# Kernel optimization log

Measured on AMD Instinct MI355X. Metric: run time of the kernel, lower is better.

Reference implementation:

```python
import jax, jax.numpy as jnp
import numpy as np

B, CIN, H, W = 4, 128, 160, 160
K = 100          # num instances
CH = 8           # mask head channels
OUT = 8          # mask branch out channels
STRIDE = 4
EPS = 1e-5


def conv3x3(x, w):
    # x: [B,C,H,W], w: [O,C,3,3] -> [B,O,H,W], stride 1, pad 1
    return jax.lax.conv_general_dilated(x, w, (1, 1), 'SAME',
                                        dimension_numbers=('NCHW', 'OIHW', 'NCHW'))


def setup_inputs() -> dict:
    key = jax.random.key(0)
    ks = jax.random.split(key, 6)
    cnn_feature = jax.random.normal(ks[0], (B, CIN, H, W), jnp.float32)
    tower_w = jax.random.normal(ks[1], (4, 128, 128, 3, 3), jnp.float32) * 0.03
    bn_gamma = jnp.ones((4, 128), jnp.float32)
    bn_beta = jnp.zeros((4, 128), jnp.float32)
    bn_mean = jnp.zeros((4, 128), jnp.float32)
    bn_var = jnp.ones((4, 128), jnp.float32)
    proj_w = jax.random.normal(ks[2], (OUT, 128), jnp.float32) * 0.05
    proj_b = jnp.zeros((OUT,), jnp.float32)
    ctrl_w = jax.random.normal(ks[3], (169, CIN, 3, 3), jnp.float32) * 0.01
    ctrl_b = jnp.zeros((169,), jnp.float32)
    detection = jax.random.randint(ks[4], (K, 2), 0, min(H, W), dtype=jnp.int32)
    return dict(cnn_feature=cnn_feature, tower_w=tower_w, bn_gamma=bn_gamma,
                bn_beta=bn_beta, bn_mean=bn_mean, bn_var=bn_var,
                proj_w=proj_w, proj_b=proj_b, ctrl_w=ctrl_w, ctrl_b=ctrl_b,
                detection=detection)


def reference(cnn_feature, tower_w, bn_gamma, bn_beta, bn_mean, bn_var,
              proj_w, proj_b, ctrl_w, ctrl_b, detection):
    x = cnn_feature
    for i in range(4):
        x = conv3x3(x, tower_w[i])
        inv = bn_gamma[i] / jnp.sqrt(bn_var[i] + EPS)            # [128]
        shift = bn_beta[i] - bn_mean[i] * inv
        x = jax.nn.relu(x * inv[None, :, None, None] + shift[None, :, None, None])
    mask_feats = jnp.einsum('bchw,oc->bohw', x, proj_w) + proj_b[None, :, None, None]

    # ----- controller: 3x3 conv producing 169 dynamic params per pixel -----
    ctrl = conv3x3(cnn_feature, ctrl_w) + ctrl_b[None, :, None, None]  # [B,169,H,W]

    # ----- gather per-instance params at detection centers (im_inds all 0) -----
    xs = detection[:, 0]
    ys = detection[:, 1]
    params = ctrl[0][:, ys, xs].T  # [K,169]

    # ----- relative coordinates -----
    sx = jnp.arange(W, dtype=jnp.float32) * STRIDE + STRIDE // 2
    sy = jnp.arange(H, dtype=jnp.float32) * STRIDE + STRIDE // 2
    gy, gx = jnp.meshgrid(sy, sx, indexing='ij')
    locations = jnp.stack([gx.reshape(-1), gy.reshape(-1)], axis=1)   # [HW,2]
    ct = detection.astype(jnp.float32) * STRIDE                        # [K,2]
    rel = (ct[:, None, :] - locations[None, :, :]).transpose(0, 2, 1)  # [K,2,HW]

    feats = jnp.broadcast_to(mask_feats[0].reshape(1, OUT, H * W), (K, OUT, H * W))
    h = jnp.concatenate([rel, feats], axis=1)  # [K,10,HW]

    # ----- parse dynamic params: weights first, then biases -----
    w0 = params[:, 0:80].reshape(K, CH, OUT + 2)     # (8+2)*8
    w1 = params[:, 80:144].reshape(K, CH, CH)        # 8*8
    w2 = params[:, 144:152].reshape(K, 1, CH)        # 8*1
    b0 = params[:, 152:160]
    b1 = params[:, 160:168]
    b2 = params[:, 168:169]

    # ----- dynamic grouped 1x1 convs == per-instance matmuls -----
    h = jax.nn.relu(jnp.einsum('koc,kcp->kop', w0, h) + b0[:, :, None])
    h = jax.nn.relu(jnp.einsum('koc,kcp->kop', w1, h) + b1[:, :, None])
    h = jnp.einsum('koc,kcp->kop', w2, h) + b2[:, :, None]  # [K,1,HW]
    return h.reshape(K, H, W)
```

## Files before the change

### kernel.cpp

```cpp
#include <hip/hip_runtime.h>
#include <hip/hip_bf16.h>

#define H 160
#define W 160
#define HW 25600
#define ROWB 40960

typedef __attribute__((ext_vector_type(8))) short bf16x8;
typedef __attribute__((ext_vector_type(4))) float f32x4;
typedef __attribute__((ext_vector_type(8))) unsigned short ushort8v;
typedef __attribute__((ext_vector_type(4))) unsigned short ushort4v;

typedef __attribute__((address_space(1))) const unsigned int gu32;
typedef __attribute__((address_space(3))) unsigned int lu32;

__device__ __forceinline__ void gload16(const void* g, void* l) {
    __builtin_amdgcn_global_load_lds((gu32*)g, (lu32*)l, 16, 0, 0);
}

__device__ __forceinline__ unsigned short f2b(float f) {
    unsigned int u = __float_as_uint(f);
    unsigned int r = (u + 0x7fffu + ((u >> 16) & 1u)) >> 16;
    return (unsigned short)r;
}
__device__ __forceinline__ float b2f(unsigned short b) {
    return __uint_as_float(((unsigned int)b) << 16);
}

#define LGKM0() asm volatile("s_waitcnt lgkmcnt(0)" ::: "memory")
#define BARRIER() asm volatile("s_barrier" ::: "memory")


__global__ __launch_bounds__(256) void prep_weights(
    const float* __restrict__ tw,
    const float* __restrict__ gamma, const float* __restrict__ beta,
    const float* __restrict__ mean,  const float* __restrict__ var,
    char* __restrict__ wbf, float* __restrict__ invshift)
{
    int idx = blockIdx.x * 256 + threadIdx.x;
    int ci = idx & 127;
    int co = (idx >> 7) & 127;
    int lt = idx >> 14;
    int l  = lt / 9;
    int tap = lt - l * 9;
    int kk = ci >> 5;
    int cw = ci & 31;
    float v = tw[(((l * 128 + co) * 128 + ci) * 9) + tap];
    *(unsigned short*)(wbf + (lt * 4 + kk) * 8192 + co * 64 + cw * 2) = f2b(v);

    if (blockIdx.x == 0) {
        for (int c = threadIdx.x; c < 512; c += 256) {
            int ll = c >> 7, ch = c & 127;
            float inv = gamma[ll * 128 + ch] * rsqrtf(var[ll * 128 + ch] + 1e-5f);
            float sh  = beta[ll * 128 + ch] - mean[ll * 128 + ch] * inv;
            invshift[ll * 256 + ch] = inv;
            invshift[ll * 256 + 128 + ch] = sh;
        }
    }
}

__global__ __launch_bounds__(256) void prep_input(
    const float* __restrict__ cnn, char* __restrict__ actX)
{
    int idx = blockIdx.x * 256 + threadIdx.x;
    int cb = idx & 15;
    int p  = idx >> 4;
    int x  = p % W;
    int key = (x & 7) << 5;
    int ci0 = cb * 8;
    ushort8v o;
#pragma unroll
    for (int j = 0; j < 8; ++j)
        o[j] = f2b(cnn[(ci0 + j) * HW + p]);
    *(ushort8v*)(actX + p * 256 + ((cb * 16) ^ key)) = o;
}

template <int PROJ>
__global__ __launch_bounds__(256, 2) void conv_mfma(
    const char* __restrict__ actin,
    const char* __restrict__ wpl,
    const float* __restrict__ invshift_l,
    char* __restrict__ actout,
    const float* __restrict__ pw,
    const float* __restrict__ pb,
    float* __restrict__ mf)
{
    __shared__ __align__(16) char smem[60416];
    char* IT = smem;
    char* WQ = smem + 27648;

    const int tid  = threadIdx.x;
    const int lane = tid & 63;
    const int wave = tid >> 6;
    const int g    = lane >> 4;
    const int i15  = lane & 15;
    const int wc   = wave >> 1;
    const int wp   = wave & 1;

    const int bx = blockIdx.x;
    const int by = blockIdx.y;
    const int tx0 = bx * 16 - 1;
    const int ty0 = by * 4 - 1;

    for (int it = 0; it < 7; ++it) {
        int c = it * 256 + tid;
        if (c < 1728) {
            int row  = c / 288;
            int rem  = c - row * 288;
            int px_i = rem >> 4;
            int bo   = (rem & 15) * 16;
            int cy = min(max(ty0 + row, 0), H - 1);
            int cx = min(max(tx0 + px_i, 0), W - 1);
            char* ldsb = IT + (it * 256 + (tid & ~63)) * 16;
            gload16(actin + cy * ROWB + cx * 256 + bo, ldsb);
        }
    }
#pragma unroll
    for (int pl = 0; pl < 3; ++pl) {
        const char* src = wpl + pl * 8192;
        char* dst = WQ + pl * 8192;
        gload16(src + (0 * 256 + tid) * 16, dst + (0 * 256 + (tid & ~63)) * 16);
        gload16(src + (1 * 256 + tid) * 16, dst + (1 * 256 + (tid & ~63)) * 16);
    }
    asm volatile("s_waitcnt vmcnt(6)" ::: "memory");
    for (int c = tid; c < 1728; c += 256) {
        int row  = c / 288;
        int rem  = c - row * 288;
        int px_i = rem >> 4;
        int gy = ty0 + row, gx = tx0 + px_i;
        if ((unsigned)gy >= (unsigned)H || (unsigned)gx >= (unsigned)W) {
            f32x4 z = {0.f, 0.f, 0.f, 0.f};
            *(f32x4*)(IT + c * 16) = z;
        }
    }
    LGKM0();
    BARRIER();

    f32x4 acc[4][2];
#pragma unroll
    for (int cf = 0; cf < 4; ++cf)
#pragma unroll
        for (int pf = 0; pf < 2; ++pf)
            acc[cf][pf] = (f32x4){0.f, 0.f, 0.f, 0.f};

#define CSTAGE(J, WN) {                                                        \
    if ((J) <= 32) {                                                           \
        const char* src = wpl + ((J) + 3) * 8192;                              \
        char* dst = WQ + (((J) + 3) & 3) * 8192;                               \
        gload16(src + (0*256 + tid) * 16, dst + (0*256 + (tid & ~63)) * 16);   \
        gload16(src + (1*256 + tid) * 16, dst + (1*256 + (tid & ~63)) * 16);   \
    }                                                                          \
    asm volatile("s_waitcnt vmcnt(" #WN ")" ::: "memory");                     \
    {                                                                          \
        const int tap = (J) >> 2, kk = (J) & 3;                                \
        const int r = tap / 3, s = tap - r * 3;                                \
        const int kb = kk * 64 + g * 16;                                       \
        const int keyb = ((i15 + s + 7) & 7) << 5;                             \
        const char* wbase = WQ + ((J) & 3) * 8192 + (wc * 64 + i15) * 64 + g * 16; \
        bf16x8 a0 = *(const bf16x8*)(wbase + 0 * 1024);                        \
        bf16x8 a1 = *(const bf16x8*)(wbase + 1 * 1024);                        \
        bf16x8 a2 = *(const bf16x8*)(wbase + 2 * 1024);                        \
        bf16x8 a3 = *(const bf16x8*)(wbase + 3 * 1024);                        \
        const char* ib = IT + (i15 + s) * 256 + (kb ^ keyb);                   \
        bf16x8 b0 = *(const bf16x8*)(ib + (wp * 2 + 0 + r) * 4608);            \
        bf16x8 b1 = *(const bf16x8*)(ib + (wp * 2 + 1 + r) * 4608);            \
        acc[0][0] = __builtin_amdgcn_mfma_f32_16x16x32_bf16(a0, b0, acc[0][0], 0, 0, 0); \
        acc[0][1] = __builtin_amdgcn_mfma_f32_16x16x32_bf16(a0, b1, acc[0][1], 0, 0, 0); \
        acc[1][0] = __builtin_amdgcn_mfma_f32_16x16x32_bf16(a1, b0, acc[1][0], 0, 0, 0); \
        acc[1][1] = __builtin_amdgcn_mfma_f32_16x16x32_bf16(a1, b1, acc[1][1], 0, 0, 0); \
        acc[2][0] = __builtin_amdgcn_mfma_f32_16x16x32_bf16(a2, b0, acc[2][0], 0, 0, 0); \
        acc[2][1] = __builtin_amdgcn_mfma_f32_16x16x32_bf16(a2, b1, acc[2][1], 0, 0, 0); \
        acc[3][0] = __builtin_amdgcn_mfma_f32_16x16x32_bf16(a3, b0, acc[3][0], 0, 0, 0); \
        acc[3][1] = __builtin_amdgcn_mfma_f32_16x16x32_bf16(a3, b1, acc[3][1], 0, 0, 0); \
    }                                                                          \
    BARRIER();                                                                 \
}

    CSTAGE(0,4)  CSTAGE(1,4)  CSTAGE(2,4)  CSTAGE(3,4)  CSTAGE(4,4)  CSTAGE(5,4)
    CSTAGE(6,4)  CSTAGE(7,4)  CSTAGE(8,4)  CSTAGE(9,4)  CSTAGE(10,4) CSTAGE(11,4)
    CSTAGE(12,4) CSTAGE(13,4) CSTAGE(14,4) CSTAGE(15,4) CSTAGE(16,4) CSTAGE(17,4)
    CSTAGE(18,4) CSTAGE(19,4) CSTAGE(20,4) CSTAGE(21,4) CSTAGE(22,4) CSTAGE(23,4)
    CSTAGE(24,4) CSTAGE(25,4) CSTAGE(26,4) CSTAGE(27,4) CSTAGE(28,4) CSTAGE(29,4)
    CSTAGE(30,4) CSTAGE(31,4) CSTAGE(32,4) CSTAGE(33,2) CSTAGE(34,0) CSTAGE(35,0)
#undef CSTAGE

    if (PROJ == 0) {
        const int gx = bx * 16 + i15;
        const int keyo = (gx & 7) << 5;
#pragma unroll
        for (int cf = 0; cf < 4; ++cf) {
            int co0 = wc * 64 + cf * 16 + g * 4;
            f32x4 inv4 = *(const f32x4*)&invshift_l[co0];
            f32x4 sh4  = *(const f32x4*)&invshift_l[128 + co0];
#pragma unroll
            for (int pf = 0; pf < 2; ++pf) {
                int gy = by * 4 + wp * 2 + pf;
                f32x4 v = acc[cf][pf];
                ushort4v o;
                o.x = f2b(fmaxf(v.x * inv4.x + sh4.x, 0.f));
                o.y = f2b(fmaxf(v.y * inv4.y + sh4.y, 0.f));
                o.z = f2b(fmaxf(v.z * inv4.z + sh4.z, 0.f));
                o.w = f2b(fmaxf(v.w * inv4.w + sh4.w, 0.f));
                *(ushort4v*)(actout + gy * ROWB + gx * 256 + ((co0 * 2) ^ keyo)) = o;
            }
        }
    } else {
        float* actF = (float*)(smem + 27648);
        float* spw  = (float*)smem;
#pragma unroll
        for (int cf = 0; cf < 4; ++cf) {
            int co0 = wc * 64 + cf * 16 + g * 4;
            f32x4 inv4 = *(const f32x4*)&invshift_l[co0];
            f32x4 sh4  = *(const f32x4*)&invshift_l[128 + co0];
#pragma unroll
            for (int pf = 0; pf < 2; ++pf) {
                int pxi = (wp * 2 + pf) * 16 + i15;
                f32x4 v = acc[cf][pf];
                f32x4 o;
                o.x = fmaxf(v.x * inv4.x + sh4.x, 0.f);
                o.y = fmaxf(v.y * inv4.y + sh4.y, 0.f);
                o.z = fmaxf(v.z * inv4.z + sh4.z, 0.f);
                o.w = fmaxf(v.w * inv4.w + sh4.w, 0.f);
                *(f32x4*)&actF[pxi * 128 + (co0 ^ ((pxi & 7) << 2))] = o;
            }
        }
        for (int i = tid; i < 1024; i += 256) spw[i] = pw[i];
        LGKM0();
        BARRIER();
        int pxt = tid >> 2;
        int o0  = (tid & 3) * 2;
        float s0 = 0.f, s1 = 0.f;
#pragma unroll
        for (int ci = 0; ci < 128; ci += 4) {
            f32x4 a  = *(const f32x4*)&actF[pxt * 128 + (ci ^ ((pxt & 7) << 2))];
            f32x4 w0 = *(const f32x4*)&spw[o0 * 128 + ci];
            f32x4 w1 = *(const f32x4*)&spw[(o0 + 1) * 128 + ci];
            s0 += a.x * w0.x + a.y * w0.y + a.z * w0.z + a.w * w0.w;
            s1 += a.x * w1.x + a.y * w1.y + a.z * w1.z + a.w * w1.w;
        }
        int p = (by * 4 + (pxt >> 4)) * W + bx * 16 + (pxt & 15);
        mf[o0 * HW + p]       = s0 + pb[o0];
        mf[(o0 + 1) * HW + p] = s1 + pb[o0 + 1];
    }
}

__global__ __launch_bounds__(256) void ctrl_kernel(
    const float* __restrict__ feat, const float* __restrict__ cw,
    const float* __restrict__ cb, const int* __restrict__ det,
    float* __restrict__ params)
{
    __shared__ float patch[1152];
    const int tid = threadIdx.x;
    const int k = blockIdx.x;
    const int xk = det[2 * k];
    const int yk = det[2 * k + 1];

    for (int i = tid; i < 1152; i += 256) {
        int ci = i / 9;
        int rem = i - ci * 9;
        int r = rem / 3, s = rem - r * 3;
        int gy = yk + r - 1, gx = xk + s - 1;
        float v = 0.f;
        if ((unsigned)gy < (unsigned)H && (unsigned)gx < (unsigned)W)
            v = feat[ci * HW + gy * W + gx];
        patch[i] = v;
    }
    __syncthreads();

    if (tid < 169) {
        float acc = cb[tid];
        const float4* cw4 = (const float4*)&cw[tid * 1152];
        const float4* p4  = (const float4*)patch;
        for (int i = 0; i < 288; ++i) {
            float4 a = p4[i];
            float4 b = cw4[i];
            acc += a.x * b.x + a.y * b.y + a.z * b.z + a.w * b.w;
        }
        params[k * 169 + tid] = acc;
    }
}

__global__ __launch_bounds__(256) void head_kernel(
    const float* __restrict__ mf, const float* __restrict__ params,
    const int* __restrict__ det, float* __restrict__ out)
{
    __shared__ float sp[1690];
    __shared__ int sdet[20];
    const int tid = threadIdx.x;
    const int kg = blockIdx.y;
    for (int i = tid; i < 1690; i += 256) sp[i] = params[kg * 1690 + i];
    if (tid < 20) sdet[tid] = det[kg * 20 + tid];
    __syncthreads();

    const int p = blockIdx.x * 256 + tid;
    const int x = p % W;
    const int y = p / W;
    const float fx = (float)(x * 4 + 2);
    const float fy = (float)(y * 4 + 2);

    float f[8];
#pragma unroll
    for (int o = 0; o < 8; ++o) f[o] = mf[o * HW + p];

#pragma unroll 2
    for (int j = 0; j < 10; ++j) {
        const float* spj = &sp[j * 169];
        const float rel0 = (float)(sdet[2 * j] * 4) - fx;
        const float rel1 = (float)(sdet[2 * j + 1] * 4) - fy;
        float h0[8];
#pragma unroll
        for (int o = 0; o < 8; ++o) {
            float a = spj[152 + o] + spj[o * 10] * rel0 + spj[o * 10 + 1] * rel1;
#pragma unroll
            for (int c = 0; c < 8; ++c) a += spj[o * 10 + 2 + c] * f[c];
            h0[o] = fmaxf(a, 0.f);
        }
        float h1[8];
#pragma unroll
        for (int o = 0; o < 8; ++o) {
            float a = spj[160 + o];
#pragma unroll
            for (int c = 0; c < 8; ++c) a += spj[80 + o * 8 + c] * h0[c];
            h1[o] = fmaxf(a, 0.f);
        }
        float r = spj[168];
#pragma unroll
        for (int c = 0; c < 8; ++c) r += spj[144 + c] * h1[c];
        out[(kg * 10 + j) * HW + p] = r;
    }
}

extern "C" void kernel_launch(void* const* d_in, const int* in_sizes, int n_in,
                              void* d_out, int out_size, void* d_ws, size_t ws_size,
                              hipStream_t stream)
{
    const float* cnn    = (const float*)d_in[0];
    const float* towerw = (const float*)d_in[1];
    const float* gamma  = (const float*)d_in[2];
    const float* beta   = (const float*)d_in[3];
    const float* meanp  = (const float*)d_in[4];
    const float* varp   = (const float*)d_in[5];
    const float* projw  = (const float*)d_in[6];
    const float* projb  = (const float*)d_in[7];
    const float* ctrlw  = (const float*)d_in[8];
    const float* ctrlb  = (const float*)d_in[9];
    const int*   det    = (const int*)d_in[10];
    float* out = (float*)d_out;

    char*  outb     = (char*)d_out;
    char*  X        = outb;
    char*  wbf      = outb + 6553600;
    float* invshift = (float*)(outb + 7733248);

    char*  Y      = (char*)d_ws;
    float* mf     = (float*)((char*)d_ws + 6553600);
    float* params = (float*)((char*)d_ws + 7372800);

    const dim3 blk(256);

    prep_weights<<<dim3(2304), blk, 0, stream>>>(towerw, gamma, beta, meanp, varp,
                                                 wbf, invshift);
    prep_input<<<dim3(1600), blk, 0, stream>>>(cnn, X);

    const dim3 cgrid(10, 40);
    conv_mfma<0><<<cgrid, blk, 0, stream>>>(X, wbf + 0 * 294912, invshift + 0 * 256,
                                            Y, nullptr, nullptr, nullptr);
    conv_mfma<0><<<cgrid, blk, 0, stream>>>(Y, wbf + 1 * 294912, invshift + 1 * 256,
                                            X, nullptr, nullptr, nullptr);
    conv_mfma<0><<<cgrid, blk, 0, stream>>>(X, wbf + 2 * 294912, invshift + 2 * 256,
                                            Y, nullptr, nullptr, nullptr);
    conv_mfma<1><<<cgrid, blk, 0, stream>>>(Y, wbf + 3 * 294912, invshift + 3 * 256,
                                            nullptr, projw, projb, mf);

    ctrl_kernel<<<dim3(100), blk, 0, stream>>>(cnn, ctrlw, ctrlb, det, params);
    head_kernel<<<dim3(100, 10), blk, 0, stream>>>(mf, params, det, out);
}
```

Before: 123.7 us.

## Split conv K-dimension across waves with per-tap weight staging and LDS reduction

The conv kernel now has each wave own a 32-channel slice of the input and compute all 128 output channels by 64 pixels. Weights for a full tap (32 KB) are staged per step, which replaces 36 fine-grained stages with 9 barriers. Partial sums are reduced across waves through LDS, and the projection epilogue is switched to bf16. This removes barrier overhead and raises MFMA density per wave, at the cost of 128 accumulator registers, dropping the 2-blocks occupancy hint, adding a reduction phase, and exposing weight loads because they are no longer double-buffered. Weight prep also loops over the 9 taps per thread with fewer blocks.

New measurement: 456.2 us. 3.69x slower.

```diff
diff --git a/kernel.cpp b/kernel.cpp
--- a/kernel.cpp
+++ b/kernel.cpp
@@ -40,13 +40,14 @@
     int idx = blockIdx.x * 256 + threadIdx.x;
     int ci = idx & 127;
     int co = (idx >> 7) & 127;
-    int lt = idx >> 14;
-    int l  = lt / 9;
-    int tap = lt - l * 9;
+    int l  = idx >> 14;
     int kk = ci >> 5;
     int cw = ci & 31;
-    float v = tw[(((l * 128 + co) * 128 + ci) * 9) + tap];
-    *(unsigned short*)(wbf + (lt * 4 + kk) * 8192 + co * 64 + cw * 2) = f2b(v);
+    const float* src = tw + ((l * 128 + co) * 128 + ci) * 9;
+    char* dst = wbf + l * 294912 + kk * 8192 + co * 64 + cw * 2;
+#pragma unroll
+    for (int t = 0; t < 9; ++t)
+        *(unsigned short*)(dst + t * 32768) = f2b(src[t]);
 
     if (blockIdx.x == 0) {
         for (int c = threadIdx.x; c < 512; c += 256) {
@@ -76,7 +77,7 @@
 }
 
 template <int PROJ>
-__global__ __launch_bounds__(256, 2) void conv_mfma(
+__global__ __launch_bounds__(256) void conv_mfma(
     const char* __restrict__ actin,
     const char* __restrict__ wpl,
     const float* __restrict__ invshift_l,
@@ -87,15 +88,13 @@
 {
     __shared__ __align__(16) char smem[60416];
     char* IT = smem;
-    char* WQ = smem + 27648;
+    char* WT = smem + 27648;
 
     const int tid  = threadIdx.x;
     const int lane = tid & 63;
-    const int wave = tid >> 6;
+    const int w    = tid >> 6;
     const int g    = lane >> 4;
     const int i15  = lane & 15;
-    const int wc   = wave >> 1;
-    const int wp   = wave & 1;
 
     const int bx = blockIdx.x;
     const int by = blockIdx.y;
@@ -116,13 +115,11 @@
         }
     }
 #pragma unroll
-    for (int pl = 0; pl < 3; ++pl) {
-        const char* src = wpl + pl * 8192;
-        char* dst = WQ + pl * 8192;
-        gload16(src + (0 * 256 + tid) * 16, dst + (0 * 256 + (tid & ~63)) * 16);
-        gload16(src + (1 * 256 + tid) * 16, dst + (1 * 256 + (tid & ~63)) * 16);
-    }
-    asm volatile("s_waitcnt vmcnt(6)" ::: "memory");
+    for (int it = 0; it < 8; ++it) {
+        int c = it * 256 + tid;
+        gload16(wpl + c * 16, WT + (it * 256 + (tid & ~63)) * 16);
+    }
+    asm volatile("s_waitcnt vmcnt(8)" ::: "memory");
     for (int c = tid; c < 1728; c += 256) {
         int row  = c / 288;
         int rem  = c - row * 288;
@@ -133,115 +130,146 @@
             *(f32x4*)(IT + c * 16) = z;
         }
     }
-    LGKM0();
-    BARRIER();
-
-    f32x4 acc[4][2];
-#pragma unroll
-    for (int cf = 0; cf < 4; ++cf)
-#pragma unroll
-        for (int pf = 0; pf < 2; ++pf)
+
+    f32x4 acc[8][4];
+#pragma unroll
+    for (int cf = 0; cf < 8; ++cf)
+#pragma unroll
+        for (int pf = 0; pf < 4; ++pf)
             acc[cf][pf] = (f32x4){0.f, 0.f, 0.f, 0.f};
 
-#define CSTAGE(J, WN) {                                                        \
-    if ((J) <= 32) {                                                           \
-        const char* src = wpl + ((J) + 3) * 8192;                              \
-        char* dst = WQ + (((J) + 3) & 3) * 8192;                               \
-        gload16(src + (0*256 + tid) * 16, dst + (0*256 + (tid & ~63)) * 16);   \
-        gload16(src + (1*256 + tid) * 16, dst + (1*256 + (tid & ~63)) * 16);   \
-    }                                                                          \
-    asm volatile("s_waitcnt vmcnt(" #WN ")" ::: "memory");                     \
-    {                                                                          \
-        const int tap = (J) >> 2, kk = (J) & 3;                                \
-        const int r = tap / 3, s = tap - r * 3;                                \
-        const int kb = kk * 64 + g * 16;                                       \
-        const int keyb = ((i15 + s + 7) & 7) << 5;                             \
-        const char* wbase = WQ + ((J) & 3) * 8192 + (wc * 64 + i15) * 64 + g * 16; \
-        bf16x8 a0 = *(const bf16x8*)(wbase + 0 * 1024);                        \
-        bf16x8 a1 = *(const bf16x8*)(wbase + 1 * 1024);                        \
-        bf16x8 a2 = *(const bf16x8*)(wbase + 2 * 1024);                        \
-        bf16x8 a3 = *(const bf16x8*)(wbase + 3 * 1024);                        \
-        const char* ib = IT + (i15 + s) * 256 + (kb ^ keyb);                   \
-        bf16x8 b0 = *(const bf16x8*)(ib + (wp * 2 + 0 + r) * 4608);            \
-        bf16x8 b1 = *(const bf16x8*)(ib + (wp * 2 + 1 + r) * 4608);            \
-        acc[0][0] = __builtin_amdgcn_mfma_f32_16x16x32_bf16(a0, b0, acc[0][0], 0, 0, 0); \
-        acc[0][1] = __builtin_amdgcn_mfma_f32_16x16x32_bf16(a0, b1, acc[0][1], 0, 0, 0); \
-        acc[1][0] = __builtin_amdgcn_mfma_f32_16x16x32_bf16(a1, b0, acc[1][0], 0, 0, 0); \
-        acc[1][1] = __builtin_amdgcn_mfma_f32_16x16x32_bf16(a1, b1, acc[1][1], 0, 0, 0); \
-        acc[2][0] = __builtin_amdgcn_mfma_f32_16x16x32_bf16(a2, b0, acc[2][0], 0, 0, 0); \
-        acc[2][1] = __builtin_amdgcn_mfma_f32_16x16x32_bf16(a2, b1, acc[2][1], 0, 0, 0); \
-        acc[3][0] = __builtin_amdgcn_mfma_f32_16x16x32_bf16(a3, b0, acc[3][0], 0, 0, 0); \
-        acc[3][1] = __builtin_amdgcn_mfma_f32_16x16x32_bf16(a3, b1, acc[3][1], 0, 0, 0); \
-    }                                                                          \
-    BARRIER();                                                                 \
-}
-
-    CSTAGE(0,4)  CSTAGE(1,4)  CSTAGE(2,4)  CSTAGE(3,4)  CSTAGE(4,4)  CSTAGE(5,4)
-    CSTAGE(6,4)  CSTAGE(7,4)  CSTAGE(8,4)  CSTAGE(9,4)  CSTAGE(10,4) CSTAGE(11,4)
-    CSTAGE(12,4) CSTAGE(13,4) CSTAGE(14,4) CSTAGE(15,4) CSTAGE(16,4) CSTAGE(17,4)
-    CSTAGE(18,4) CSTAGE(19,4) CSTAGE(20,4) CSTAGE(21,4) CSTAGE(22,4) CSTAGE(23,4)
-    CSTAGE(24,4) CSTAGE(25,4) CSTAGE(26,4) CSTAGE(27,4) CSTAGE(28,4) CSTAGE(29,4)
-    CSTAGE(30,4) CSTAGE(31,4) CSTAGE(32,4) CSTAGE(33,2) CSTAGE(34,0) CSTAGE(35,0)
-#undef CSTAGE
-
-    if (PROJ == 0) {
-        const int gx = bx * 16 + i15;
-        const int keyo = (gx & 7) << 5;
-#pragma unroll
-        for (int cf = 0; cf < 4; ++cf) {
-            int co0 = wc * 64 + cf * 16 + g * 4;
-            f32x4 inv4 = *(const f32x4*)&invshift_l[co0];
-            f32x4 sh4  = *(const f32x4*)&invshift_l[128 + co0];
-#pragma unroll
-            for (int pf = 0; pf < 2; ++pf) {
-                int gy = by * 4 + wp * 2 + pf;
-                f32x4 v = acc[cf][pf];
-                ushort4v o;
-                o.x = f2b(fmaxf(v.x * inv4.x + sh4.x, 0.f));
-                o.y = f2b(fmaxf(v.y * inv4.y + sh4.y, 0.f));
-                o.z = f2b(fmaxf(v.z * inv4.z + sh4.z, 0.f));
-                o.w = f2b(fmaxf(v.w * inv4.w + sh4.w, 0.f));
-                *(ushort4v*)(actout + gy * ROWB + gx * 256 + ((co0 * 2) ^ keyo)) = o;
-            }
-        }
-    } else {
-        float* actF = (float*)(smem + 27648);
-        float* spw  = (float*)smem;
-#pragma unroll
-        for (int cf = 0; cf < 4; ++cf) {
-            int co0 = wc * 64 + cf * 16 + g * 4;
-            f32x4 inv4 = *(const f32x4*)&invshift_l[co0];
-            f32x4 sh4  = *(const f32x4*)&invshift_l[128 + co0];
-#pragma unroll
-            for (int pf = 0; pf < 2; ++pf) {
-                int pxi = (wp * 2 + pf) * 16 + i15;
-                f32x4 v = acc[cf][pf];
-                f32x4 o;
-                o.x = fmaxf(v.x * inv4.x + sh4.x, 0.f);
-                o.y = fmaxf(v.y * inv4.y + sh4.y, 0.f);
-                o.z = fmaxf(v.z * inv4.z + sh4.z, 0.f);
-                o.w = fmaxf(v.w * inv4.w + sh4.w, 0.f);
-                *(f32x4*)&actF[pxi * 128 + (co0 ^ ((pxi & 7) << 2))] = o;
-            }
-        }
-        for (int i = tid; i < 1024; i += 256) spw[i] = pw[i];
+    const int kb = w * 64 + g * 16;
+
+#pragma unroll
+    for (int tap = 0; tap < 9; ++tap) {
+        asm volatile("s_waitcnt vmcnt(0)" ::: "memory");
         LGKM0();
         BARRIER();
-        int pxt = tid >> 2;
-        int o0  = (tid & 3) * 2;
+        {
+            const int r = tap / 3, s = tap - r * 3;
+            const int keyb = ((i15 + s + 7) & 7) << 5;
+            const char* wb = WT + w * 8192 + i15 * 64 + g * 16;
+            bf16x8 a[8];
+#pragma unroll
+            for (int cf = 0; cf < 8; ++cf)
+                a[cf] = *(const bf16x8*)(wb + cf * 1024);
+            const char* ib = IT + (i15 + s) * 256 + (kb ^ keyb);
+            bf16x8 b[4];
+#pragma unroll
+            for (int pf = 0; pf < 4; ++pf)
+                b[pf] = *(const bf16x8*)(ib + (pf + r) * 4608);
+#pragma unroll
+            for (int cf = 0; cf < 8; ++cf)
+#pragma unroll
+                for (int pf = 0; pf < 4; ++pf)
+                    acc[cf][pf] = __builtin_amdgcn_mfma_f32_16x16x32_bf16(
+                        a[cf], b[pf], acc[cf][pf], 0, 0, 0);
+        }
+        BARRIER();
+        if (tap < 8) {
+            const char* wtap = wpl + (tap + 1) * 32768;
+#pragma unroll
+            for (int it = 0; it < 8; ++it) {
+                int c = it * 256 + tid;
+                gload16(wtap + c * 16, WT + (it * 256 + (tid & ~63)) * 16);
+            }
+        }
+    }
+
+    char* redA = smem + 27648;
+    char* redB = smem + 27648 + 16384;
+    const int swz = (i15 & 7) << 4;
+#define REDAB(buf, pfi, cf) ((buf) + ((pfi) * 16 + i15) * 512 + (((cf) * 64 + g * 16) ^ swz))
+    if (w == 2) { for (int cf = 0; cf < 8; ++cf) { *(f32x4*)REDAB(redA,0,cf) = acc[cf][0]; *(f32x4*)REDAB(redA,1,cf) = acc[cf][1]; } }
+    if (w == 3) { for (int cf = 0; cf < 8; ++cf) { *(f32x4*)REDAB(redB,0,cf) = acc[cf][0]; *(f32x4*)REDAB(redB,1,cf) = acc[cf][1]; } }
+    __syncthreads();
+    if (w == 0) { for (int cf = 0; cf < 8; ++cf) { acc[cf][0] += *(f32x4*)REDAB(redA,0,cf); acc[cf][1] += *(f32x4*)REDAB(redA,1,cf); } }
+    if (w == 1) { for (int cf = 0; cf < 8; ++cf) { acc[cf][0] += *(f32x4*)REDAB(redB,0,cf); acc[cf][1] += *(f32x4*)REDAB(redB,1,cf); } }
+    __syncthreads();
+    if (w == 2) { for (int cf = 0; cf < 8; ++cf) { *(f32x4*)REDAB(redA,0,cf) = acc[cf][2]; *(f32x4*)REDAB(redA,1,cf) = acc[cf][3]; } }
+    if (w == 3) { for (int cf = 0; cf < 8; ++cf) { *(f32x4*)REDAB(redB,0,cf) = acc[cf][2]; *(f32x4*)REDAB(redB,1,cf) = acc[cf][3]; } }
+    __syncthreads();
+    if (w == 0) { for (int cf = 0; cf < 8; ++cf) { acc[cf][2] += *(f32x4*)REDAB(redA,0,cf); acc[cf][3] += *(f32x4*)REDAB(redA,1,cf); } }
+    if (w == 1) { for (int cf = 0; cf < 8; ++cf) { acc[cf][2] += *(f32x4*)REDAB(redB,0,cf); acc[cf][3] += *(f32x4*)REDAB(redB,1,cf); } }
+    __syncthreads();
+#define REDC(buf, pf, cfq) ((buf) + ((pf) * 16 + i15) * 256 + (((cfq) * 64 + g * 16) ^ swz))
+    if (w == 1) { for (int cf = 0; cf < 4; ++cf) for (int pf = 0; pf < 4; ++pf) *(f32x4*)REDC(redA, pf, cf) = acc[cf][pf]; }
+    if (w == 0) { for (int cf = 4; cf < 8; ++cf) for (int pf = 0; pf < 4; ++pf) *(f32x4*)REDC(redB, pf, (cf - 4)) = acc[cf][pf]; }
+    __syncthreads();
+    if (w == 0) { for (int cf = 0; cf < 4; ++cf) for (int pf = 0; pf < 4; ++pf) acc[cf][pf] += *(f32x4*)REDC(redA, pf, cf); }
+    if (w == 1) { for (int cf = 4; cf < 8; ++cf) for (int pf = 0; pf < 4; ++pf) acc[cf][pf] += *(f32x4*)REDC(redB, pf, (cf - 4)); }
+
+    if (PROJ == 0) {
+        if (w < 2) {
+            const int gx = bx * 16 + i15;
+            const int keyo = (gx & 7) << 5;
+            const int cf0 = w * 4;
+#pragma unroll
+            for (int cfq = 0; cfq < 4; ++cfq) {
+                int cf = cf0 + cfq;
+                int co0 = cf * 16 + g * 4;
+                f32x4 inv4 = *(const f32x4*)&invshift_l[co0];
+                f32x4 sh4  = *(const f32x4*)&invshift_l[128 + co0];
+#pragma unroll
+                for (int pf = 0; pf < 4; ++pf) {
+                    int gy = by * 4 + pf;
+                    f32x4 v = acc[cf][pf];
+                    ushort4v o;
+                    o.x = f2b(fmaxf(v.x * inv4.x + sh4.x, 0.f));
+                    o.y = f2b(fmaxf(v.y * inv4.y + sh4.y, 0.f));
+                    o.z = f2b(fmaxf(v.z * inv4.z + sh4.z, 0.f));
+                    o.w = f2b(fmaxf(v.w * inv4.w + sh4.w, 0.f));
+                    *(ushort4v*)(actout + gy * ROWB + gx * 256 + ((co0 * 2) ^ keyo)) = o;
+                }
+            }
+        }
+    } else {
+        char* actF = smem;
+        float* spw = (float*)(smem + 16384);
+        for (int i = tid; i < 1024; i += 256) spw[i] = pw[i];
+        if (w < 2) {
+            const int cf0 = w * 4;
+#pragma unroll
+            for (int cfq = 0; cfq < 4; ++cfq) {
+                int cf = cf0 + cfq;
+                int co0 = cf * 16 + g * 4;
+                f32x4 inv4 = *(const f32x4*)&invshift_l[co0];
+                f32x4 sh4  = *(const f32x4*)&invshift_l[128 + co0];
+#pragma unroll
+                for (int pf = 0; pf < 4; ++pf) {
+                    int px = pf * 16 + i15;
+                    f32x4 v = acc[cf][pf];
+                    ushort4v o;
+                    o.x = f2b(fmaxf(v.x * inv4.x + sh4.x, 0.f));
+                    o.y = f2b(fmaxf(v.y * inv4.y + sh4.y, 0.f));
+                    o.z = f2b(fmaxf(v.z * inv4.z + sh4.z, 0.f));
+                    o.w = f2b(fmaxf(v.w * inv4.w + sh4.w, 0.f));
+                    *(ushort4v*)(actF + px * 256 + ((co0 * 2) ^ ((px & 7) << 5))) = o;
+                }
+            }
+        }
+        __syncthreads();
+        int px = tid & 63;
+        int o0 = (tid >> 6) * 2;
+        int key = (px & 7) << 5;
         float s0 = 0.f, s1 = 0.f;
 #pragma unroll
-        for (int ci = 0; ci < 128; ci += 4) {
-            f32x4 a  = *(const f32x4*)&actF[pxt * 128 + (ci ^ ((pxt & 7) << 2))];
-            f32x4 w0 = *(const f32x4*)&spw[o0 * 128 + ci];
-            f32x4 w1 = *(const f32x4*)&spw[(o0 + 1) * 128 + ci];
-            s0 += a.x * w0.x + a.y * w0.y + a.z * w0.z + a.w * w0.w;
-            s1 += a.x * w1.x + a.y * w1.y + a.z * w1.z + a.w * w1.w;
-        }
-        int p = (by * 4 + (pxt >> 4)) * W + bx * 16 + (pxt & 15);
+        for (int cb = 0; cb < 16; ++cb) {
+            ushort8v vv = *(const ushort8v*)(actF + px * 256 + ((cb * 16) ^ key));
+#pragma unroll
+            for (int j = 0; j < 8; ++j) {
+                float f = b2f(vv[j]);
+                int ci = cb * 8 + j;
+                s0 += f * spw[o0 * 128 + ci];
+                s1 += f * spw[(o0 + 1) * 128 + ci];
+            }
+        }
+        int p = (by * 4 + (px >> 4)) * W + bx * 16 + (px & 15);
         mf[o0 * HW + p]       = s0 + pb[o0];
         mf[(o0 + 1) * HW + p] = s1 + pb[o0 + 1];
     }
+#undef REDAB
+#undef REDC
 }
 
 __global__ __launch_bounds__(256) void ctrl_kernel(
@@ -358,8 +386,8 @@
 
     const dim3 blk(256);
 
-    prep_weights<<<dim3(2304), blk, 0, stream>>>(towerw, gamma, beta, meanp, varp,
-                                                 wbf, invshift);
+    prep_weights<<<dim3(256), blk, 0, stream>>>(towerw, gamma, beta, meanp, varp,
+                                                wbf, invshift);
     prep_input<<<dim3(1600), blk, 0, stream>>>(cnn, X);
 
     const dim3 cgrid(10, 40);
```
